# Performance work log

Measured on AMD Instinct MI355X. Metric: run time of the kernel, lower is better.

The kernel has to match this reference:

```python
import jax, jax.numpy as jnp
import numpy as np

FP8_E4M3_MAX = 448.0
BLOCK_SIZE = 128


def _block_quant_dequant_e4m3(x, block_size=BLOCK_SIZE):
    """Per-block (along last dim) FP8 E4M3 fake quantize: returns dequantized fp32."""
    M, K = x.shape
    nb = K // block_size
    xb = x.reshape(M, nb, block_size)
    amax = jnp.clip(jnp.max(jnp.abs(xb), axis=-1, keepdims=True), 1e-12, None)
    scale = FP8_E4M3_MAX / amax  # per-block scale, [M, nb, 1]
    q = jnp.clip(xb * scale, -FP8_E4M3_MAX, FP8_E4M3_MAX).astype(jnp.float8_e4m3fn)
    deq = q.astype(jnp.float32) / scale
    return deq.reshape(M, K)


def _dual_quantize_weight(w, block_size=BLOCK_SIZE):
    """TCFP-12 dual quantization: FP8 hi component + FP8-quantized residual (lo)."""
    w_hi = _block_quant_dequant_e4m3(w, block_size)
    residual = w - w_hi
    w_lo = _block_quant_dequant_e4m3(residual, block_size)
    return w_hi + w_lo


def setup_inputs() -> dict:
    key = jax.random.key(0)
    k1, k2, k3 = jax.random.split(key, 3)
    B, T, DIN, DOUT = 8, 4096, 1024, 1024
    x = jax.random.normal(k1, (B, T, DIN), dtype=jnp.float32)
    weight = jax.random.normal(k2, (DOUT, DIN), dtype=jnp.float32) * 0.02
    bias = jax.random.normal(k3, (DOUT,), dtype=jnp.float32) * 0.01
    return {"x": x, "weight": weight, "bias": bias}


def reference(x, weight, bias):
    # Block-quantize activations (fake-quant, per 128-col block, E4M3)
    B, T, DIN = x.shape
    x2d = x.reshape(-1, DIN)
    x_q = _block_quant_dequant_e4m3(x2d, BLOCK_SIZE)
    # Dual-quantize weight: hi + residual lo components
    w_q = _dual_quantize_weight(weight, BLOCK_SIZE)
    # Block-scaled GEMM (dequantized reference math) + bias
    out2d = x_q @ w_q.T + bias
    return out2d.reshape(B, T, -1)
```

## Files before the change

kernel.cpp:

```cpp
#include <hip/hip_runtime.h>
#include <hip/hip_bf16.h>

typedef __bf16 bf16x8 __attribute__((ext_vector_type(8)));
typedef float  f32x4  __attribute__((ext_vector_type(4)));

#define GLOAD_LDS16(gptr, lptr)                                                  \
  __builtin_amdgcn_global_load_lds(                                              \
      (const __attribute__((address_space(1))) void*)(gptr),                     \
      (__attribute__((address_space(3))) void*)(lptr), 16, 0, 0)

__device__ __forceinline__ unsigned short f2bf(float f) {
  __hip_bfloat16 h = __float2bfloat16(f);
  return __builtin_bit_cast(unsigned short, h);
}

__device__ __forceinline__ void fq4(float* __restrict__ v) {
  float am = fmaxf(fmaxf(fabsf(v[0]), fabsf(v[1])),
                   fmaxf(fabsf(v[2]), fabsf(v[3])));
  am = fmaxf(am, __shfl_xor(am, 1));
  am = fmaxf(am, __shfl_xor(am, 2));
  am = fmaxf(am, __shfl_xor(am, 4));
  am = fmaxf(am, __shfl_xor(am, 8));
  am = fmaxf(am, __shfl_xor(am, 16));
  am = fmaxf(am, 1e-12f);
  const float scale = 448.0f / am;
  const float inv   = am * (1.0f / 448.0f);
  float c0 = fminf(fmaxf(v[0] * scale, -448.0f), 448.0f);
  float c1 = fminf(fmaxf(v[1] * scale, -448.0f), 448.0f);
  float c2 = fminf(fmaxf(v[2] * scale, -448.0f), 448.0f);
  float c3 = fminf(fmaxf(v[3] * scale, -448.0f), 448.0f);
  int pk = __builtin_amdgcn_cvt_pk_fp8_f32(c0, c1, 0, false);
  pk = __builtin_amdgcn_cvt_pk_fp8_f32(c2, c3, pk, true);
  v[0] = __builtin_amdgcn_cvt_f32_fp8(pk, 0) * inv;
  v[1] = __builtin_amdgcn_cvt_f32_fp8(pk, 1) * inv;
  v[2] = __builtin_amdgcn_cvt_f32_fp8(pk, 2) * inv;
  v[3] = __builtin_amdgcn_cvt_f32_fp8(pk, 3) * inv;
}

__global__ __launch_bounds__(256) void quant_x_k(const float* __restrict__ x,
                                                 unsigned short* __restrict__ xq) {
  const size_t u = (size_t)blockIdx.x * 256 + threadIdx.x;
  float v[4];
  *(float4*)v = ((const float4*)x)[u];
  fq4(v);
  union { uint2 q; unsigned short s[4]; } pk;
#pragma unroll
  for (int e = 0; e < 4; ++e) pk.s[e] = f2bf(v[e]);
  ((uint2*)xq)[u] = pk.q;
}

__global__ __launch_bounds__(256) void quant_w_k(const float* __restrict__ w,
                                                 unsigned short* __restrict__ wq) {
  const size_t u = (size_t)blockIdx.x * 256 + threadIdx.x;
  float a[4], h[4], r[4];
  *(float4*)a = ((const float4*)w)[u];
#pragma unroll
  for (int i = 0; i < 4; ++i) h[i] = a[i];
  fq4(h);
#pragma unroll
  for (int i = 0; i < 4; ++i) r[i] = a[i] - h[i];
  fq4(r);
  union { uint2 q; unsigned short s[4]; } pk;
#pragma unroll
  for (int e = 0; e < 4; ++e) pk.s[e] = f2bf(h[e] + r[e]);
  ((uint2*)wq)[u] = pk.q;
}

#define BM 128
#define BN 128
#define BK 64

__global__ __launch_bounds__(256) void gemm_bt_bias(
    const unsigned short* __restrict__ A,
    const unsigned short* __restrict__ B,
    const float* __restrict__ bias,
    float* __restrict__ C,
    int M, int N, int K) {
  __shared__ unsigned short ldsA[2 * BM * BK];
  __shared__ unsigned short ldsB[2 * BN * BK];

  const int tid  = threadIdx.x;
  const int wave = tid >> 6;
  const int lane = tid & 63;
  const int nbn  = N / BN;
  const int nbm  = M / BM;

  int bm, bn;
  if ((nbm & 7) == 0) {
    const int xcd = blockIdx.x & 7;
    const int j   = blockIdx.x >> 3;
    bn = j % nbn;
    bm = xcd * (nbm >> 3) + j / nbn;
  } else {
    bn = blockIdx.x % nbn;
    bm = blockIdx.x / nbn;
  }

  const int wr = wave >> 1;
  const int wc = wave & 1;

  f32x4 acc[4][4] = {};

  const int rload = wave * 32 + (lane >> 3);
  const int cload = (((lane & 7) ^ (lane >> 3)) * 8);
  const unsigned short* gA = A + (size_t)(bm * BM + rload) * K + cload;
  const unsigned short* gB = B + (size_t)(bn * BN + rload) * K + cload;
  unsigned short* lA = ldsA + wave * 2048 + lane * 8;
  unsigned short* lB = ldsB + wave * 2048 + lane * 8;

  auto stage = [&](int it, int buf) {
    const unsigned short* pA = gA + (size_t)it * BK;
    const unsigned short* pB = gB + (size_t)it * BK;
    unsigned short* dA = lA + buf * (BM * BK);
    unsigned short* dB = lB + buf * (BN * BK);
#pragma unroll
    for (int t = 0; t < 4; ++t) {
      GLOAD_LDS16(pA + (size_t)(t * 8) * K, dA + t * 512);
      GLOAD_LDS16(pB + (size_t)(t * 8) * K, dB + t * 512);
    }
  };

  auto compute = [&](const unsigned short* bA, const unsigned short* bB) {
    const int fRow = lane & 15;
    const int sw   = fRow & 7;
#pragma unroll
    for (int kc = 0; kc < 2; ++kc) {
      const int c    = kc * 4 + (lane >> 4);
      const int sOff = ((c ^ sw) * 8);
      bf16x8 af[4], bfr[4];
#pragma unroll
      for (int i = 0; i < 4; ++i)
        af[i] = *(const bf16x8*)&bA[(wr * 64 + i * 16 + fRow) * BK + sOff];
#pragma unroll
      for (int j = 0; j < 4; ++j)
        bfr[j] = *(const bf16x8*)&bB[(wc * 64 + j * 16 + fRow) * BK + sOff];
#pragma unroll
      for (int i = 0; i < 4; ++i)
#pragma unroll
        for (int j = 0; j < 4; ++j)
          acc[i][j] = __builtin_amdgcn_mfma_f32_16x16x32_bf16(af[i], bfr[j],
                                                              acc[i][j], 0, 0, 0);
    }
  };

  stage(0, 0);
  const int niter = K / BK;
  for (int it = 0; it < niter; it += 2) {
    __syncthreads();
    if (it + 1 < niter) stage(it + 1, 1);
    compute(ldsA, ldsB);
    __syncthreads();
    if (it + 2 < niter) stage(it + 2, 0);
    compute(ldsA + BM * BK, ldsB + BN * BK);
  }

  const int    n0 = bn * BN + wc * 64 + (lane & 15);
  const size_t m0 = (size_t)bm * BM + wr * 64 + ((lane >> 4) << 2);
#pragma unroll
  for (int j = 0; j < 4; ++j) {
    const int col = n0 + j * 16;
    const float bv = bias[col];
#pragma unroll
    for (int i = 0; i < 4; ++i) {
      const size_t base = (m0 + (size_t)i * 16) * N + col;
#pragma unroll
      for (int r = 0; r < 4; ++r)
        C[base + (size_t)r * N] = acc[i][j][r] + bv;
    }
  }
}

extern "C" void kernel_launch(void* const* d_in, const int* in_sizes, int n_in,
                              void* d_out, int out_size, void* d_ws, size_t ws_size,
                              hipStream_t stream) {
  const float* x    = (const float*)d_in[0];
  const float* w    = (const float*)d_in[1];
  const float* bias = (const float*)d_in[2];

  const int DOUT = in_sizes[2];
  const int DIN  = in_sizes[1] / DOUT;
  const int M    = in_sizes[0] / DIN;

  unsigned short* xq = (unsigned short*)d_ws;
  unsigned short* wq = xq + (size_t)M * DIN;

  hipLaunchKernelGGL(quant_x_k, dim3((size_t)M * DIN / 4 / 256), dim3(256), 0,
                     stream, x, xq);
  hipLaunchKernelGGL(quant_w_k, dim3((size_t)DOUT * DIN / 4 / 256), dim3(256), 0,
                     stream, w, wq);

  const int grid = (M / BM) * (DOUT / BN);
  hipLaunchKernelGGL(gemm_bt_bias, dim3(grid), dim3(256), 0, stream,
                     xq, wq, bias, (float*)d_out, M, DOUT, DIN);
}
```

Before: 306.7 us.

## Rewrite GEMM as 256x256 tile, 8-wave ping-pong pipeline with fine-grained waits

```diff
diff --git a/kernel.cpp b/kernel.cpp
--- a/kernel.cpp
+++ b/kernel.cpp
@@ -66,21 +66,29 @@
   ((uint2*)wq)[u] = pk.q;
 }
 
-#define BM 128
-#define BN 128
+#define BM 256
+#define BN 256
 #define BK 64
 
-__global__ __launch_bounds__(256) void gemm_bt_bias(
+#define VM4()  asm volatile("s_waitcnt vmcnt(4)" ::: "memory")
+#define VM2()  asm volatile("s_waitcnt vmcnt(2)" ::: "memory")
+#define VM0()  asm volatile("s_waitcnt vmcnt(0)" ::: "memory")
+#define LG0()  do { asm volatile("s_waitcnt lgkmcnt(0)" ::: "memory");           \
+                    __builtin_amdgcn_sched_barrier(0); } while (0)
+#define BAR()  __builtin_amdgcn_s_barrier()
+
+__global__ __launch_bounds__(512, 2) void gemm_bt_bias(
     const unsigned short* __restrict__ A,
     const unsigned short* __restrict__ B,
     const float* __restrict__ bias,
     float* __restrict__ C,
     int M, int N, int K) {
-  __shared__ unsigned short ldsA[2 * BM * BK];
-  __shared__ unsigned short ldsB[2 * BN * BK];
+  __shared__ unsigned short lds[65536];
+  unsigned short* ldsA = lds;
+  unsigned short* ldsB = lds + 32768;
 
   const int tid  = threadIdx.x;
-  const int wave = tid >> 6;
+  const int wv   = tid >> 6;
   const int lane = tid & 63;
   const int nbn  = N / BN;
   const int nbm  = M / BM;
@@ -96,76 +104,131 @@
     bm = blockIdx.x / nbn;
   }
 
-  const int wr = wave >> 1;
-  const int wc = wave & 1;
-
-  f32x4 acc[4][4] = {};
-
-  const int rload = wave * 32 + (lane >> 3);
-  const int cload = (((lane & 7) ^ (lane >> 3)) * 8);
-  const unsigned short* gA = A + (size_t)(bm * BM + rload) * K + cload;
-  const unsigned short* gB = B + (size_t)(bn * BN + rload) * K + cload;
-  unsigned short* lA = ldsA + wave * 2048 + lane * 8;
-  unsigned short* lB = ldsB + wave * 2048 + lane * 8;
-
-  auto stage = [&](int it, int buf) {
-    const unsigned short* pA = gA + (size_t)it * BK;
-    const unsigned short* pB = gB + (size_t)it * BK;
-    unsigned short* dA = lA + buf * (BM * BK);
-    unsigned short* dB = lB + buf * (BN * BK);
-#pragma unroll
-    for (int t = 0; t < 4; ++t) {
-      GLOAD_LDS16(pA + (size_t)(t * 8) * K, dA + t * 512);
-      GLOAD_LDS16(pB + (size_t)(t * 8) * K, dB + t * 512);
-    }
-  };
-
-  auto compute = [&](const unsigned short* bA, const unsigned short* bB) {
-    const int fRow = lane & 15;
-    const int sw   = fRow & 7;
-#pragma unroll
-    for (int kc = 0; kc < 2; ++kc) {
-      const int c    = kc * 4 + (lane >> 4);
-      const int sOff = ((c ^ sw) * 8);
-      bf16x8 af[4], bfr[4];
-#pragma unroll
-      for (int i = 0; i < 4; ++i)
-        af[i] = *(const bf16x8*)&bA[(wr * 64 + i * 16 + fRow) * BK + sOff];
-#pragma unroll
-      for (int j = 0; j < 4; ++j)
-        bfr[j] = *(const bf16x8*)&bB[(wc * 64 + j * 16 + fRow) * BK + sOff];
-#pragma unroll
-      for (int i = 0; i < 4; ++i)
-#pragma unroll
-        for (int j = 0; j < 4; ++j)
-          acc[i][j] = __builtin_amdgcn_mfma_f32_16x16x32_bf16(af[i], bfr[j],
-                                                              acc[i][j], 0, 0, 0);
-    }
-  };
-
-  stage(0, 0);
-  const int niter = K / BK;
-  for (int it = 0; it < niter; it += 2) {
-    __syncthreads();
-    if (it + 1 < niter) stage(it + 1, 1);
-    compute(ldsA, ldsB);
-    __syncthreads();
-    if (it + 2 < niter) stage(it + 2, 0);
-    compute(ldsA + BM * BK, ldsB + BN * BK);
-  }
-
-  const int    n0 = bn * BN + wc * 64 + (lane & 15);
-  const size_t m0 = (size_t)bm * BM + wr * 64 + ((lane >> 4) << 2);
-#pragma unroll
-  for (int j = 0; j < 4; ++j) {
-    const int col = n0 + j * 16;
+  const int wr = wv >> 2;
+  const int wc = wv & 3;
+
+  f32x4  acc[8][4] = {};
+  bf16x8 a[4][2], b01[2][2], b23[2][2];
+
+  const int    srcChunk = ((lane & 7) ^ ((lane >> 3) & 7)) * 8;
+  const size_t laneSrc  = (size_t)(lane >> 3) * K + srcChunk;
+  const unsigned short* gA = A + (size_t)bm * BM * K + laneSrc;
+  const unsigned short* gB = B + (size_t)bn * BN * K + laneSrc;
+  const int lr0 = wv * 16, lr1 = wv * 16 + 8;
+  auto arow = [](int mq, int lr) { return mq * 64 + (lr < 64 ? lr : 64 + lr); };
+  auto brow = [](int v,  int lr) { return v * 32 + (lr >> 5) * 64 + (lr & 31); };
+  const int rA[2][2] = {{arow(0, lr0), arow(0, lr1)}, {arow(1, lr0), arow(1, lr1)}};
+  const int rB[2][2] = {{brow(0, lr0), brow(0, lr1)}, {brow(1, lr0), brow(1, lr1)}};
+
+  auto stageA = [&](int buf, int mq, int kt) {
+#pragma unroll
+    for (int t = 0; t < 2; ++t) {
+      const int rb = rA[mq][t];
+      GLOAD_LDS16(gA + (size_t)rb * K + kt * BK,
+                  ldsA + buf * 16384 + rb * 64 + lane * 8);
+    }
+  };
+  auto stageB = [&](int buf, int v, int kt) {
+#pragma unroll
+    for (int t = 0; t < 2; ++t) {
+      const int rb = rB[v][t];
+      GLOAD_LDS16(gB + (size_t)rb * K + kt * BK,
+                  ldsB + buf * 16384 + rb * 64 + lane * 8);
+    }
+  };
+
+  const int fRow = lane & 15;
+  const int q4   = lane >> 4;
+  const int s8   = fRow & 7;
+  const int sw0  = ((q4)     ^ s8) * 8;
+  const int sw1  = ((4 + q4) ^ s8) * 8;
+  const int aRO  = (wr * 128 + fRow) * 64;
+  const int bRO  = (wc * 64  + fRow) * 64;
+
+  auto dsA = [&](int buf, int mq) {
+    const unsigned short* p = ldsA + buf * 16384 + aRO + mq * 4096;
+#pragma unroll
+    for (int m = 0; m < 4; ++m) {
+      a[m][0] = *(const bf16x8*)(p + m * 1024 + sw0);
+      a[m][1] = *(const bf16x8*)(p + m * 1024 + sw1);
+    }
+  };
+  auto dsB = [&](int buf, int njp, bf16x8 (&bb)[2][2]) {
+    const unsigned short* p = ldsB + buf * 16384 + bRO + njp * 2048;
+#pragma unroll
+    for (int n = 0; n < 2; ++n) {
+      bb[n][0] = *(const bf16x8*)(p + n * 1024 + sw0);
+      bb[n][1] = *(const bf16x8*)(p + n * 1024 + sw1);
+    }
+  };
+
+  auto mm = [&](int mq, int njp, bf16x8 (&bb)[2][2]) {
+    __builtin_amdgcn_s_setprio(1);
+#pragma unroll
+    for (int m = 0; m < 4; ++m)
+#pragma unroll
+      for (int n = 0; n < 2; ++n)
+#pragma unroll
+        for (int k = 0; k < 2; ++k)
+          acc[mq * 4 + m][njp * 2 + n] = __builtin_amdgcn_mfma_f32_16x16x32_bf16(
+              a[m][k], bb[n][k], acc[mq * 4 + m][njp * 2 + n], 0, 0, 0);
+    __builtin_amdgcn_s_setprio(0);
+  };
+
+  stageA(0, 0, 0); stageB(0, 0, 0); stageB(0, 1, 0); stageA(0, 1, 0);
+  VM4(); BAR();
+
+  const int niter = K / (2 * BK);
+  for (int i = 0; i < niter - 1; ++i) {
+    const int t1 = 2 * i + 1, t2 = 2 * i + 2;
+    dsA(0, 0); dsB(0, 0, b01); stageA(1, 0, t1);
+    BAR(); LG0(); mm(0, 0, b01); VM4(); BAR();
+    dsB(0, 1, b23); stageB(1, 0, t1);
+    BAR(); LG0(); mm(0, 1, b23); VM4(); BAR();
+    dsA(0, 1); stageB(1, 1, t1);
+    BAR(); LG0(); mm(1, 0, b01); BAR();
+    stageA(1, 1, t1);
+    BAR(); mm(1, 1, b23); VM4(); BAR();
+    dsA(1, 0); dsB(1, 0, b01); stageA(0, 0, t2);
+    BAR(); LG0(); mm(0, 0, b01); VM4(); BAR();
+    dsB(1, 1, b23); stageB(0, 0, t2);
+    BAR(); LG0(); mm(0, 1, b23); VM4(); BAR();
+    dsA(1, 1); stageB(0, 1, t2);
+    BAR(); LG0(); mm(1, 0, b01); BAR();
+    stageA(0, 1, t2);
+    BAR(); mm(1, 1, b23); VM4(); BAR();
+  }
+  {
+    const int t1 = 2 * niter - 1;
+    dsA(0, 0); dsB(0, 0, b01); stageA(1, 0, t1);
+    BAR(); LG0(); mm(0, 0, b01); VM4(); BAR();
+    dsB(0, 1, b23); stageB(1, 0, t1);
+    BAR(); LG0(); mm(0, 1, b23); VM4(); BAR();
+    dsA(0, 1); stageB(1, 1, t1);
+    BAR(); LG0(); mm(1, 0, b01); BAR();
+    stageA(1, 1, t1);
+    BAR(); mm(1, 1, b23); VM4(); BAR();
+    dsA(1, 0); dsB(1, 0, b01);
+    BAR(); LG0(); mm(0, 0, b01); VM2(); BAR();
+    dsB(1, 1, b23);
+    BAR(); LG0(); mm(0, 1, b23); VM0(); BAR();
+    dsA(1, 1);
+    BAR(); LG0(); mm(1, 0, b01); BAR();
+    mm(1, 1, b23);
+  }
+
+  const int    n0 = bn * BN + wc * 64 + fRow;
+  const size_t m0 = (size_t)bm * BM + wr * 128 + (q4 << 2);
+#pragma unroll
+  for (int nj = 0; nj < 4; ++nj) {
+    const int col = n0 + nj * 16;
     const float bv = bias[col];
 #pragma unroll
-    for (int i = 0; i < 4; ++i) {
-      const size_t base = (m0 + (size_t)i * 16) * N + col;
+    for (int mi = 0; mi < 8; ++mi) {
+      const size_t base = (m0 + (size_t)mi * 16) * N + col;
 #pragma unroll
       for (int r = 0; r < 4; ++r)
-        C[base + (size_t)r * N] = acc[i][j][r] + bv;
+        C[base + (size_t)r * N] = acc[mi][nj][r] + bv;
     }
   }
 }
@@ -190,6 +253,6 @@
                      stream, w, wq);
 
   const int grid = (M / BM) * (DOUT / BN);
-  hipLaunchKernelGGL(gemm_bt_bias, dim3(grid), dim3(256), 0, stream,
+  hipLaunchKernelGGL(gemm_bt_bias, dim3(grid), dim3(512), 0, stream,
                      xq, wq, bias, (float*)d_out, M, DOUT, DIN);
 }
```

Measured after the change: 307.6 us. About the same (+0.3%).
